# Optimization experiments

Hardware: AMD Instinct MI355X
Metric: run time of the kernel (lower is better)

The kernel has to match this reference:

```python
import jax, jax.numpy as jnp
import numpy as np

EPS = 1e-5
C = 512


def conv1x1(x, w, b):
    # 1x1 conv == per-pixel linear: x [B,C,H,W], w [O,C], b [O]
    return jnp.einsum('bchw,oc->bohw', x, w) + b[None, :, None, None]


def mean_variance_norm(feat):
    # per (batch, channel) normalization over spatial dims, unbiased var + eps
    b, c, h, w = feat.shape
    flat = feat.reshape(b, c, h * w)
    mean = flat.mean(axis=2)[:, :, None, None]
    std = jnp.sqrt(jnp.var(flat, axis=2, ddof=1) + EPS)[:, :, None, None]
    return (feat - mean) / std


def setup_inputs() -> dict:
    key = jax.random.key(0)
    ks = jax.random.split(key, 10)
    sc = 1.0 / np.sqrt(C)
    inp = {
        'content': jax.random.normal(ks[0], (2, C, 64, 64), jnp.float32),
        'style': jax.random.normal(ks[1], (2, C, 64, 64), jnp.float32),
        'f_w': jax.random.normal(ks[2], (C, C), jnp.float32) * sc,
        'f_b': jnp.zeros((C,), jnp.float32),
        'g_w': jax.random.normal(ks[3], (C, C), jnp.float32) * sc,
        'g_b': jnp.zeros((C,), jnp.float32),
        'h_w': jax.random.normal(ks[4], (C, C), jnp.float32) * sc,
        'h_b': jnp.zeros((C,), jnp.float32),
        'out_w': jax.random.normal(ks[5], (C, C), jnp.float32) * sc,
        'out_b': jnp.zeros((C,), jnp.float32),
    }
    return inp


def reference(content, style, f_w, f_b, g_w, g_b, h_w, h_b, out_w, out_b):
    b, c, h, w = content.shape
    Fq = conv1x1(content, f_w, f_b).reshape(b, c, h * w).transpose(0, 2, 1)  # [b,Nc,C]
    Gk = conv1x1(style, g_w, g_b).reshape(b, c, -1)                           # [b,C,Ns]
    Hv = conv1x1(style, h_w, h_b).reshape(b, c, -1).transpose(0, 2, 1)        # [b,Ns,C]

    S = jax.nn.softmax(jnp.einsum('bnc,bcs->bns', Fq, Gk), axis=-1)           # [b,Nc,Ns]
    mean = jnp.einsum('bns,bsc->bnc', S, Hv)                                   # E[x]
    second = jnp.einsum('bns,bsc->bnc', S, Hv * Hv)                            # E[x^2]
    std = jnp.sqrt(jnp.maximum(second - mean * mean, 0.0))

    mean = mean.reshape(b, h, w, c).transpose(0, 3, 1, 2)
    std = std.reshape(b, h, w, c).transpose(0, 3, 1, 2)

    O = std * mean_variance_norm(content) + mean
    O = conv1x1(O, out_w, out_b)
    return O + content
```

## Files before the change

### kernel.cpp

```cpp
#include <hip/hip_runtime.h>
#include <math.h>

#define NS 4096
#define CH 512
#define EPSV 1e-5f

typedef __attribute__((ext_vector_type(8))) _Float16 f16x8;
typedef __attribute__((ext_vector_type(4))) float f32x4;
typedef unsigned short u16;

__device__ __forceinline__ u16 f2h(float x) {
    _Float16 h = (_Float16)x;
    return __builtin_bit_cast(unsigned short, h);
}
__device__ __forceinline__ float h2f(u16 b) {
    return (float)__builtin_bit_cast(_Float16, b);
}

__device__ __forceinline__ void gload16(const void* g, void* l) {
    __builtin_amdgcn_global_load_lds((const __attribute__((address_space(1))) unsigned*)g,
                                     (__attribute__((address_space(3))) unsigned*)l, 16, 0, 0);
}

struct ZTab {
    long aoff[8];
    long boff[8];
    long ooff[8];
    long coff[8];
    int  mode[8];
    int  np[8];
    const float* bias[8];
};

struct PA4 { const float* w[4]; };
struct PB2 { const float* x[2]; };

template<int NPZ, bool GS>
__device__ __forceinline__ void kloop(
    const u16* __restrict__ pAhi, const u16* __restrict__ pAlo,
    const u16* __restrict__ pBhi,
    u16* smem, int smemStride,
    int Mw, int Nw, int K, int m0, int n0,
    int wid, int lane, int lk, int lm, int wm, int wn,
    const float* __restrict__ cbase,
    f32x4 (&acc)[4][4])
{
    auto stage = [&](int buf, int ks) {
        const int kp0 = ks << 2;
        #pragma unroll
        for (int i = 0; i < 2 * NPZ; ++i) {
            const int q = i * 4 + wid;
            const int b = q >> 3;
            const int p = (q & 7) >> 1;
            const int w = ((q & 1) << 6) + lane;
            const u16* src;
            if (b == 0)      src = pAhi + ((size_t)(kp0 + p) * Mw + m0 + w) * 8;
            else if (b == 1) src = pBhi + ((size_t)(kp0 + p) * Nw + n0 + w) * 8;
            else             src = pAlo + ((size_t)(kp0 + p) * Mw + m0 + w) * 8;
            gload16(src, &smem[(size_t)buf * smemStride + (size_t)(((b * 4 + p) * 128) + w) * 8]);
        }
    };

    const int nK = K >> 5;
    stage(0, 0);
    __syncthreads();
    int cur = 0;
    _Float16 ch[4] = {};
    for (int ks = 0; ks < nK; ++ks) {
        if (GS && (ks & 3) == 0) {
            const int g = ks >> 2;
            #pragma unroll
            for (int j = 0; j < 4; ++j)
                ch[j] = (_Float16)cbase[(size_t)g * NS + n0 + wn * 64 + j * 16 + lm];
        }
        if (ks + 1 < nK) stage(cur ^ 1, ks + 1);
        const u16* sm = smem + (size_t)cur * smemStride;
        f16x8 ah[4], bh[4], al[4];
        #pragma unroll
        for (int f = 0; f < 4; ++f) {
            ah[f] = *(const f16x8*)&sm[((0 * 4 + lk) * 128 + wm * 64 + f * 16 + lm) * 8];
            bh[f] = *(const f16x8*)&sm[((1 * 4 + lk) * 128 + wn * 64 + f * 16 + lm) * 8];
            if (GS) bh[f] = bh[f] * ch[f];
            if (NPZ == 3)
                al[f] = *(const f16x8*)&sm[((2 * 4 + lk) * 128 + wm * 64 + f * 16 + lm) * 8];
        }
        #pragma unroll
        for (int i = 0; i < 4; ++i)
            #pragma unroll
            for (int j = 0; j < 4; ++j) {
                acc[i][j] = __builtin_amdgcn_mfma_f32_16x16x32_f16(ah[i], bh[j], acc[i][j], 0, 0, 0);
                if (NPZ == 3)
                    acc[i][j] = __builtin_amdgcn_mfma_f32_16x16x32_f16(al[i], bh[j], acc[i][j], 0, 0, 0);
            }
        __syncthreads();
        cur ^= 1;
    }
}

template<int NP, bool RESID, bool COLST, bool GS>
__global__ __launch_bounds__(256, (NP == 2 ? 4 : 3)) void gemm_split(
    const u16* __restrict__ Ahi, const u16* __restrict__ Alo,
    const u16* __restrict__ Bhi,
    const float* __restrict__ resid,
    float* __restrict__ outF, u16* __restrict__ outH,
    float* __restrict__ pmg, float* __restrict__ psg,
    const float* __restrict__ cb,
    int Mw, int Nw, int K, ZTab tab)
{
    __shared__ u16 smem[2][NP * 4 * 128 * 8];
    const int t = threadIdx.x;
    const int lane = t & 63;
    const int wid = t >> 6;
    const int wm = wid >> 1, wn = wid & 1;
    const int lk = lane >> 4, lm = lane & 15;
    const int m0 = blockIdx.y * 128, n0 = blockIdx.x * 128;
    const int z = blockIdx.z;
    const int npz = tab.np[z];
    const u16* pAhi = Ahi + tab.aoff[z];
    const u16* pAlo = Alo + tab.aoff[z];
    const u16* pBhi = Bhi + tab.boff[z];
    const float* cbase = GS ? (cb + tab.coff[z]) : nullptr;

    f32x4 acc[4][4] = {};
    const int smemStride = NP * 4 * 128 * 8;

    if constexpr (NP == 2) {
        kloop<2, GS>(pAhi, pAlo, pBhi, &smem[0][0], smemStride,
                     Mw, Nw, K, m0, n0, wid, lane, lk, lm, wm, wn, cbase, acc);
    } else {
        if (npz == 2)
            kloop<2, GS>(pAhi, pAlo, pBhi, &smem[0][0], smemStride,
                         Mw, Nw, K, m0, n0, wid, lane, lk, lm, wm, wn, cbase, acc);
        else
            kloop<3, GS>(pAhi, pAlo, pBhi, &smem[0][0], smemStride,
                         Mw, Nw, K, m0, n0, wid, lane, lk, lm, wm, wn, cbase, acc);
    }

    const float* bp = tab.bias[z];
    if (COLST) {
        float* smx = (float*)&smem[0][0];
        float* ssm = smx + 256;
        #pragma unroll
        for (int j = 0; j < 4; ++j) {
            float mx = -3.0e38f;
            #pragma unroll
            for (int i = 0; i < 4; ++i)
                #pragma unroll
                for (int r = 0; r < 4; ++r)
                    mx = fmaxf(mx, acc[i][j][r]);
            mx = fmaxf(mx, __shfl_xor(mx, 16));
            mx = fmaxf(mx, __shfl_xor(mx, 32));
            float sum = 0.f;
            #pragma unroll
            for (int i = 0; i < 4; ++i)
                #pragma unroll
                for (int r = 0; r < 4; ++r)
                    sum += __expf(acc[i][j][r] - mx);
            sum += __shfl_xor(sum, 16);
            sum += __shfl_xor(sum, 32);
            if (lk == 0) {
                const int nloc = wn * 64 + j * 16 + lm;
                smx[wm * 128 + nloc] = mx;
                ssm[wm * 128 + nloc] = sum;
            }
        }
        __syncthreads();
        float mxc[4];
        #pragma unroll
        for (int j = 0; j < 4; ++j) {
            const int nloc = wn * 64 + j * 16 + lm;
            const float m0v = smx[nloc], m1v = smx[128 + nloc];
            const float mc = fmaxf(m0v, m1v);
            mxc[j] = mc;
            if (wm == 0 && lk == 0) {
                const float sc = ssm[nloc] * __expf(m0v - mc) + ssm[128 + nloc] * __expf(m1v - mc);
                const int n = n0 + nloc;
                const size_t gi = ((size_t)z * 32 + (m0 >> 7)) * NS + n;
                pmg[gi] = mc;
                psg[gi] = sc;
            }
        }
        u16* ph = outH + tab.ooff[z];
        #pragma unroll
        for (int i = 0; i < 4; ++i) {
            const long rg = (long)((m0 + wm * 64) >> 3) + i * 2 + (lk >> 1);
            const int sub = (lk & 1) * 4;
            #pragma unroll
            for (int j = 0; j < 4; ++j) {
                const int n = n0 + wn * 64 + j * 16 + lm;
                const long idx = (rg * Nw + n) * 8 + sub;
                u16 h[4];
                #pragma unroll
                for (int r = 0; r < 4; ++r)
                    h[r] = f2h(__expf(acc[i][j][r] - mxc[j]));
                *(ushort4*)&ph[idx] = make_ushort4(h[0], h[1], h[2], h[3]);
            }
        }
    } else if (tab.mode[z] == 0) {
        float* pout = outF + tab.ooff[z];
        #pragma unroll
        for (int i = 0; i < 4; ++i) {
            #pragma unroll
            for (int r = 0; r < 4; ++r) {
                const int m = m0 + wm * 64 + i * 16 + lk * 4 + r;
                const float bv = bp ? bp[m] : 0.f;
                const size_t ro = (size_t)m * Nw + n0 + wn * 64 + lm;
                #pragma unroll
                for (int j = 0; j < 4; ++j) {
                    float v = acc[i][j][r] + bv;
                    if (RESID) v += resid[tab.ooff[z] + ro + j * 16];
                    pout[ro + j * 16] = v;
                }
            }
        }
    } else {
        u16* ph = outH + tab.ooff[z];
        #pragma unroll
        for (int i = 0; i < 4; ++i) {
            float bv[4];
            #pragma unroll
            for (int r = 0; r < 4; ++r) {
                const int m = m0 + wm * 64 + i * 16 + lk * 4 + r;
                bv[r] = bp ? bp[m] : 0.f;
            }
            const long rg = (long)((m0 + wm * 64) >> 3) + i * 2 + (lk >> 1);
            const int sub = (lk & 1) * 4;
            #pragma unroll
            for (int j = 0; j < 4; ++j) {
                const int n = n0 + wn * 64 + j * 16 + lm;
                const long idx = (rg * Nw + n) * 8 + sub;
                u16 h[4];
                #pragma unroll
                for (int r = 0; r < 4; ++r)
                    h[r] = f2h(acc[i][j][r] + bv[r]);
                *(ushort4*)&ph[idx] = make_ushort4(h[0], h[1], h[2], h[3]);
            }
        }
    }
}

__global__ __launch_bounds__(256) void packB4(PB2 xs, u16* __restrict__ Hi)
{
    const int n = blockIdx.x * 256 + threadIdx.x;
    const int p = blockIdx.y;
    const int z = blockIdx.z;
    const size_t KN = (size_t)CH * NS;
    const float* Xp = xs.x[z >> 1] + (size_t)(z & 1) * KN + ((size_t)p * 8) * NS + n;
    u16 hi[8];
    #pragma unroll
    for (int j = 0; j < 8; ++j)
        hi[j] = f2h(Xp[(size_t)j * NS]);
    const size_t o = (size_t)z * KN + ((size_t)p * NS + n) * 8;
    *(uint4*)&Hi[o] = *(const uint4*)hi;
}

__global__ __launch_bounds__(256) void packA4(PA4 ws, u16* __restrict__ Hi)
{
    __shared__ float tile[64][65];
    const int t = threadIdx.x;
    const int k0 = blockIdx.x * 64, m0 = blockIdx.y * 64;
    const float* W = ws.w[blockIdx.z];
    u16* H = Hi + (size_t)blockIdx.z * CH * CH;
    const int kk = t & 63, mb = t >> 6;
    #pragma unroll
    for (int it = 0; it < 16; ++it) {
        int mm = mb + it * 4;
        tile[mm][kk] = W[(size_t)(m0 + mm) * CH + k0 + kk];
    }
    __syncthreads();
    #pragma unroll
    for (int cc = 0; cc < 2; ++cc) {
        int c = t + cc * 256;
        int kp = c >> 6, m = c & 63;
        u16 hi[8];
        #pragma unroll
        for (int j = 0; j < 8; ++j)
            hi[j] = f2h(tile[m][kp * 8 + j]);
        size_t o = ((size_t)(k0 / 8 + kp) * CH + m0 + m) * 8;
        *(uint4*)&H[o] = *(const uint4*)hi;
    }
}

__global__ __launch_bounds__(256) void pack_hvT(const float* __restrict__ Hv,
    u16* __restrict__ H1h, u16* __restrict__ H2h, u16* __restrict__ H2l)
{
    __shared__ float tile[64][65];
    const int t = threadIdx.x;
    const int s0 = blockIdx.x * 64, c0 = blockIdx.y * 64;
    const int z = blockIdx.z;
    const float* src = Hv + (size_t)z * CH * NS;
    const int ss = t & 63, cb = t >> 6;
    #pragma unroll
    for (int it = 0; it < 16; ++it) {
        int cc = cb + it * 4;
        tile[cc][ss] = src[(size_t)(c0 + cc) * NS + s0 + ss];
    }
    __syncthreads();
    const size_t zb = (size_t)z * NS * CH;
    #pragma unroll
    for (int cc2 = 0; cc2 < 2; ++cc2) {
        int c = t + cc2 * 256;
        int sp = c >> 6, cm = c & 63;
        u16 h1[8], h2[8], l2[8];
        #pragma unroll
        for (int j = 0; j < 8; ++j) {
            float v = tile[cm][sp * 8 + j];
            u16 a = f2h(v);
            h1[j] = a;
            float q = h2f(a);
            float q2 = q * q;
            u16 b = f2h(q2);
            h2[j] = b;
            l2[j] = f2h(q2 - h2f(b));
        }
        size_t o = zb + ((size_t)(s0 / 8 + sp) * CH + c0 + cm) * 8;
        *(uint4*)&H1h[o] = *(const uint4*)h1;
        *(uint4*)&H2h[o] = *(const uint4*)h2;
        *(uint4*)&H2l[o] = *(const uint4*)l2;
    }
}

__global__ __launch_bounds__(256) void colstats_comb32(const float* __restrict__ pm,
    const float* __restrict__ ps, float* __restrict__ ctab)
{
    const int n = blockIdx.x * 256 + threadIdx.x;
    const int z = blockIdx.y;
    float m = -3.0e38f, s = 0.f;
    #pragma unroll 8
    for (int g = 0; g < 32; ++g) {
        float gm = pm[((size_t)z * 32 + g) * NS + n], gs = ps[((size_t)z * 32 + g) * NS + n];
        float nm = fmaxf(m, gm);
        s = s * __expf(m - nm) + gs * __expf(gm - nm);
        m = nm;
    }
    const float inv = 1.f / s;
    #pragma unroll 8
    for (int g = 0; g < 32; ++g) {
        const size_t gi = ((size_t)z * 32 + g) * NS + n;
        ctab[gi] = __expf(pm[gi] - m) * inv;
    }
}

__global__ __launch_bounds__(256) void content_stats(const float* __restrict__ content,
                                                     float* __restrict__ cmean,
                                                     float* __restrict__ cinv)
{
    const int bc = blockIdx.x;
    const float4* p = (const float4*)(content + (size_t)bc * NS);
    const int t = threadIdx.x;
    float s = 0.f, s2 = 0.f;
    #pragma unroll
    for (int j = 0; j < 4; ++j) {
        float4 v = p[t + j * 256];
        s  += (v.x + v.y) + (v.z + v.w);
        s2 += (v.x * v.x + v.y * v.y) + (v.z * v.z + v.w * v.w);
    }
    #pragma unroll
    for (int off = 32; off >= 1; off >>= 1) {
        s  += __shfl_xor(s, off);
        s2 += __shfl_xor(s2, off);
    }
    __shared__ float r1[4], r2[4];
    const int wid = t >> 6;
    if ((t & 63) == 0) { r1[wid] = s; r2[wid] = s2; }
    __syncthreads();
    if (t == 0) {
        s  = (r1[0] + r1[1]) + (r1[2] + r1[3]);
        s2 = (r2[0] + r2[1]) + (r2[2] + r2[3]);
        const float mean = s * (1.0f / 4096.f);
        const float var = (s2 - 4096.f * mean * mean) * (1.0f / 4095.f);
        cmean[bc] = mean;
        cinv[bc] = rsqrtf(fmaxf(var, 0.f) + EPSV);
    }
}

__global__ __launch_bounds__(256) void compute_O_pack(
    const float* __restrict__ MS,
    const float* __restrict__ content,
    const float* __restrict__ cmean, const float* __restrict__ cinv,
    u16* __restrict__ Oh)
{
    const int n  = blockIdx.x * 256 + threadIdx.x;
    const int cg = blockIdx.y;
    const int b  = blockIdx.z;
    const size_t KN = (size_t)CH * NS;
    u16 h[8];
    #pragma unroll
    for (int j = 0; j < 8; ++j) {
        const int c = cg * 8 + j;
        const size_t po = (size_t)b * KN + (size_t)c * NS + n;
        const float mn = MS[po] + MS[po + 4 * KN];
        const float sc = MS[po + 2 * KN] + MS[po + 6 * KN];
        const float ct = content[po];
        const int bc = b * CH + c;
        const float o = sqrtf(fmaxf(sc - mn * mn, 0.f)) * ((ct - cmean[bc]) * cinv[bc]) + mn;
        h[j] = f2h(o);
    }
    const size_t off = (size_t)b * KN + ((size_t)cg * NS + n) * 8;
    *(uint4*)&Oh[off] = *(const uint4*)h;
}

extern "C" void kernel_launch(void* const* d_in, const int* in_sizes, int n_in,
                              void* d_out, int out_size, void* d_ws, size_t ws_size,
                              hipStream_t stream)
{
    const float* content = (const float*)d_in[0];
    const float* style   = (const float*)d_in[1];
    const float* f_w   = (const float*)d_in[2];
    const float* f_b   = (const float*)d_in[3];
    const float* g_w   = (const float*)d_in[4];
    const float* g_b   = (const float*)d_in[5];
    const float* h_w   = (const float*)d_in[6];
    const float* h_b   = (const float*)d_in[7];
    const float* out_w = (const float*)d_in[8];
    const float* out_b = (const float*)d_in[9];
    float* out = (float*)d_out;

    char* ws = (char*)d_ws;
    size_t off = 0;
    auto alloc = [&](size_t bytes) -> void* {
        void* p = ws + off;
        off = (off + bytes + 255) & ~(size_t)255;
        return p;
    };

    const size_t KN   = (size_t)CH * NS;
    const size_t CHCH = (size_t)CH * CH;
    const long   NSNS = (long)NS * NS;

    u16* Wh0 = (u16*)alloc(4 * CHCH * 2);

    u16* R2 = (u16*)alloc(6 * KN * 2);
    u16* Xc_hi = R2;
    u16* HvT_hi  = R2;
    u16* Hv2T_hi = R2 + 2 * KN;
    u16* Hv2T_lo = R2 + 4 * KN;
    (void)HvT_hi;

    u16* Fqp_hi = (u16*)alloc(2 * KN * 2);
    u16* Gkp_hi = (u16*)alloc(2 * KN * 2);
    u16* Op_hi  = Gkp_hi;

    char* R5 = (char*)alloc(2 * (size_t)NS * NS * 2);
    float* Hv32 = (float*)(R5 + 4 * KN * 4);
    u16*   E16  = (u16*)R5;

    float* MS = (float*)alloc(8 * KN * 4);

    float* pm    = (float*)alloc(2 * 32 * NS * 4);
    float* ps    = (float*)alloc(2 * 32 * NS * 4);
    float* ctab  = (float*)alloc(2 * 32 * NS * 4);
    float* cmean = (float*)alloc(1024 * 4);
    float* cinv  = (float*)alloc(1024 * 4);
    (void)ws_size; (void)in_sizes; (void)n_in; (void)out_size;

    {
        PA4 pa = { { f_w, g_w, h_w, out_w } };
        packA4<<<dim3(8, 8, 4), 256, 0, stream>>>(pa, Wh0);
        PB2 pb = { { content, style } };
        packB4<<<dim3(16, 64, 4), 256, 0, stream>>>(pb, Xc_hi);
    }
    content_stats<<<1024, 256, 0, stream>>>(content, cmean, cinv);

    {
        ZTab tb = {};
        const float* bs[3] = { f_b, g_b, h_b };
        for (int z = 0; z < 6; ++z) {
            const int w = z >> 1, b = z & 1;
            tb.aoff[z] = (long)w * CHCH;
            tb.boff[z] = (w == 0 ? 0 : (long)(2 * KN)) + (long)b * KN;
            tb.mode[z] = (w < 2) ? 1 : 0;
            tb.np[z]   = 2;
            tb.ooff[z] = (w < 2) ? ((long)w * 2 * KN + (long)b * KN)
                                 : ((long)4 * KN + (long)b * KN);
            tb.bias[z] = bs[w];
        }
        gemm_split<2, false, false, false><<<dim3(32, 4, 6), 256, 0, stream>>>(
            Wh0, nullptr, Xc_hi, nullptr,
            (float*)R5, Fqp_hi, nullptr, nullptr, nullptr, CH, NS, CH, tb);
    }

    pack_hvT<<<dim3(64, 8, 2), 256, 0, stream>>>(Hv32, R2, Hv2T_hi, Hv2T_lo);

    {
        ZTab tq = {};
        for (int z = 0; z < 2; ++z) {
            tq.aoff[z] = (long)z * KN;
            tq.boff[z] = (long)z * KN;
            tq.ooff[z] = (long)z * NSNS;
            tq.np[z]   = 2;
        }
        gemm_split<2, false, true, false><<<dim3(32, 32, 2), 256, 0, stream>>>(
            Gkp_hi, nullptr, Fqp_hi, nullptr,
            nullptr, E16, pm, ps, nullptr, NS, NS, CH, tq);
    }
    colstats_comb32<<<dim3(16, 2), 256, 0, stream>>>(pm, ps, ctab);

    {
        ZTab tp = {};
        for (int z = 0; z < 8; ++z) {
            const int p = z >> 2, sec = (z >> 1) & 1, b = z & 1;
            tp.aoff[z] = (long)sec * 2 * KN + (long)b * KN + (long)p * (KN / 2);
            tp.boff[z] = (long)b * NSNS + (long)p * (NSNS / 2);
            tp.ooff[z] = (long)p * 4 * KN + (long)sec * 2 * KN + (long)b * KN;
            tp.coff[z] = (long)b * 32 * NS + (long)p * 16 * NS;
            tp.np[z]   = sec ? 3 : 2;
        }
        gemm_split<3, false, false, true><<<dim3(32, 4, 8), 256, 0, stream>>>(
            R2, R2 + 2 * KN, E16, nullptr,
            MS, nullptr, nullptr, nullptr, ctab, CH, NS, NS / 2, tp);
    }

    compute_O_pack<<<dim3(16, 64, 2), 256, 0, stream>>>(
        MS, content, cmean, cinv, Op_hi);

    {
        ZTab tf = {};
        for (int z = 0; z < 2; ++z) {
            tf.aoff[z] = (long)3 * CHCH;
            tf.ooff[z] = (long)z * KN;
            tf.boff[z] = (long)z * KN;
            tf.np[z]   = 2;
            tf.bias[z] = out_b;
        }
        gemm_split<2, true, false, false><<<dim3(32, 4, 2), 256, 0, stream>>>(
            Wh0, nullptr, Op_hi, content,
            out, nullptr, nullptr, nullptr, nullptr, CH, NS, CH, tf);
    }
}
```

Measured before the change: 234.4 us.

## Fuse mean and second-moment PV GEMMs to share the softmax-weight B tile

Replaces the generic split GEMM that ran the E[x] and E[x^2] products as separate grid slices with a dedicated kernel. Each block loads the exponentiated score tile once, scales it by the column normalisation, and feeds it to three MFMA streams (Hv, Hv2 hi, Hv2 lo), writing both outputs. This halves the reads of the large NSxNS score matrix and the column-scaling work. In exchange it uses more accumulator registers and more LDS per block, with launch bounds set to two blocks per CU, and the grid has half as many blocks.

```diff
diff --git a/kernel.cpp b/kernel.cpp
--- a/kernel.cpp
+++ b/kernel.cpp
@@ -239,6 +239,100 @@
     }
 }
 
+__global__ __launch_bounds__(256, 2) void gemm_pv(
+    const u16* __restrict__ A1, const u16* __restrict__ A2h, const u16* __restrict__ A2l,
+    const u16* __restrict__ Bhi,
+    float* __restrict__ outF, const float* __restrict__ cb,
+    int K, ZTab tab)
+{
+    __shared__ u16 smem[2][4 * 4 * 128 * 8];
+    const int t = threadIdx.x;
+    const int lane = t & 63;
+    const int wid = t >> 6;
+    const int wm = wid >> 1, wn = wid & 1;
+    const int lk = lane >> 4, lm = lane & 15;
+    const int m0 = blockIdx.y * 128, n0 = blockIdx.x * 128;
+    const int z = blockIdx.z;
+    const u16* pA1  = A1  + tab.aoff[z];
+    const u16* pA2h = A2h + tab.aoff[z];
+    const u16* pA2l = A2l + tab.aoff[z];
+    const u16* pB   = Bhi + tab.boff[z];
+    const float* cbase = cb + tab.coff[z];
+    const int smemStride = 4 * 4 * 128 * 8;
+
+    auto stage = [&](int buf, int ks) {
+        const int kp0 = ks << 2;
+        #pragma unroll
+        for (int i = 0; i < 8; ++i) {
+            const int q = i * 4 + wid;
+            const int b = q >> 3;
+            const int p = (q & 7) >> 1;
+            const int w = ((q & 1) << 6) + lane;
+            const u16* src;
+            if (b == 0)      src = pA1  + ((size_t)(kp0 + p) * CH + m0 + w) * 8;
+            else if (b == 1) src = pB   + ((size_t)(kp0 + p) * NS + n0 + w) * 8;
+            else if (b == 2) src = pA2h + ((size_t)(kp0 + p) * CH + m0 + w) * 8;
+            else             src = pA2l + ((size_t)(kp0 + p) * CH + m0 + w) * 8;
+            gload16(src, &smem[buf][(size_t)(((b * 4 + p) * 128) + w) * 8]);
+        }
+    };
+
+    f32x4 accM[4][4] = {};
+    f32x4 accS[4][4] = {};
+
+    const int nK = K >> 5;
+    stage(0, 0);
+    __syncthreads();
+    int cur = 0;
+    _Float16 ch[4] = {};
+    for (int ks = 0; ks < nK; ++ks) {
+        if ((ks & 3) == 0) {
+            const int g = ks >> 2;
+            #pragma unroll
+            for (int j = 0; j < 4; ++j)
+                ch[j] = (_Float16)cbase[(size_t)g * NS + n0 + wn * 64 + j * 16 + lm];
+        }
+        if (ks + 1 < nK) stage(cur ^ 1, ks + 1);
+        const u16* sm = smem[cur];
+        f16x8 a1[4], bh[4], a2h[4], a2l[4];
+        #pragma unroll
+        for (int f = 0; f < 4; ++f) {
+            a1[f]  = *(const f16x8*)&sm[((0 * 4 + lk) * 128 + wm * 64 + f * 16 + lm) * 8];
+            bh[f]  = *(const f16x8*)&sm[((1 * 4 + lk) * 128 + wn * 64 + f * 16 + lm) * 8];
+            bh[f]  = bh[f] * ch[f];
+            a2h[f] = *(const f16x8*)&sm[((2 * 4 + lk) * 128 + wm * 64 + f * 16 + lm) * 8];
+            a2l[f] = *(const f16x8*)&sm[((3 * 4 + lk) * 128 + wm * 64 + f * 16 + lm) * 8];
+        }
+        #pragma unroll
+        for (int i = 0; i < 4; ++i)
+            #pragma unroll
+            for (int j = 0; j < 4; ++j) {
+                accM[i][j] = __builtin_amdgcn_mfma_f32_16x16x32_f16(a1[i],  bh[j], accM[i][j], 0, 0, 0);
+                accS[i][j] = __builtin_amdgcn_mfma_f32_16x16x32_f16(a2h[i], bh[j], accS[i][j], 0, 0, 0);
+                accS[i][j] = __builtin_amdgcn_mfma_f32_16x16x32_f16(a2l[i], bh[j], accS[i][j], 0, 0, 0);
+            }
+        __syncthreads();
+        cur ^= 1;
+    }
+
+    const size_t KN = (size_t)CH * NS;
+    float* poutM = outF + tab.ooff[z];
+    float* poutS = poutM + 2 * KN;
+    #pragma unroll
+    for (int i = 0; i < 4; ++i) {
+        #pragma unroll
+        for (int r = 0; r < 4; ++r) {
+            const int m = m0 + wm * 64 + i * 16 + lk * 4 + r;
+            const size_t ro = (size_t)m * NS + n0 + wn * 64 + lm;
+            #pragma unroll
+            for (int j = 0; j < 4; ++j) {
+                poutM[ro + j * 16] = accM[i][j][r];
+                poutS[ro + j * 16] = accS[i][j][r];
+            }
+        }
+    }
+}
+
 __global__ __launch_bounds__(256) void packB4(PB2 xs, u16* __restrict__ Hi)
 {
     const int n = blockIdx.x * 256 + threadIdx.x;
@@ -432,10 +526,8 @@
 
     u16* R2 = (u16*)alloc(6 * KN * 2);
     u16* Xc_hi = R2;
-    u16* HvT_hi  = R2;
     u16* Hv2T_hi = R2 + 2 * KN;
     u16* Hv2T_lo = R2 + 4 * KN;
-    (void)HvT_hi;
 
     u16* Fqp_hi = (u16*)alloc(2 * KN * 2);
     u16* Gkp_hi = (u16*)alloc(2 * KN * 2);
@@ -498,17 +590,15 @@
 
     {
         ZTab tp = {};
-        for (int z = 0; z < 8; ++z) {
-            const int p = z >> 2, sec = (z >> 1) & 1, b = z & 1;
-            tp.aoff[z] = (long)sec * 2 * KN + (long)b * KN + (long)p * (KN / 2);
+        for (int z = 0; z < 4; ++z) {
+            const int p = z >> 1, b = z & 1;
+            tp.aoff[z] = (long)b * KN + (long)p * (KN / 2);
             tp.boff[z] = (long)b * NSNS + (long)p * (NSNS / 2);
-            tp.ooff[z] = (long)p * 4 * KN + (long)sec * 2 * KN + (long)b * KN;
+            tp.ooff[z] = (long)p * 4 * KN + (long)b * KN;
             tp.coff[z] = (long)b * 32 * NS + (long)p * 16 * NS;
-            tp.np[z]   = sec ? 3 : 2;
-        }
-        gemm_split<3, false, false, true><<<dim3(32, 4, 8), 256, 0, stream>>>(
-            R2, R2 + 2 * KN, E16, nullptr,
-            MS, nullptr, nullptr, nullptr, ctab, CH, NS, NS / 2, tp);
+        }
+        gemm_pv<<<dim3(32, 4, 4), 256, 0, stream>>>(
+            R2, Hv2T_hi, Hv2T_lo, E16, MS, ctab, NS / 2, tp);
     }
 
     compute_O_pack<<<dim3(16, 64, 2), 256, 0, stream>>>(
```

New measurement: 212.2 us. 1.1x faster.
